# Performance work log

Hardware: AMD Instinct MI355X
Metric: run time of the kernel (lower is better)

## Reference

```python
import jax, jax.numpy as jnp
import numpy as np
import math

N = 50000
E = 800000
HID = 128
HEADS = 8
DK = HID // HEADS
EPS_LN = 1e-5


def setup_inputs() -> dict:
    key = jax.random.key(0)
    ks = jax.random.split(key, 20)
    s = 1.0 / math.sqrt(HID)
    inp = {
        'x': jax.random.normal(ks[0], (N, HID), jnp.float32),
        'Wq': jax.random.normal(ks[1], (HID, HID), jnp.float32) * s,
        'bq': jnp.zeros((HID,), jnp.float32),
        'Wk': jax.random.normal(ks[2], (HID, HID), jnp.float32) * s,
        'bk': jnp.zeros((HID,), jnp.float32),
        'Wv': jax.random.normal(ks[3], (HID, HID), jnp.float32) * s,
        'bv': jnp.zeros((HID,), jnp.float32),
        'Wo': jax.random.normal(ks[4], (HID, HID), jnp.float32) * s,
        'bo': jnp.zeros((HID,), jnp.float32),
        'ln1_g': jnp.ones((HID,), jnp.float32),
        'ln1_b': jnp.zeros((HID,), jnp.float32),
        'W1': jax.random.normal(ks[5], (HID, 4 * HID), jnp.float32) * s,
        'b1': jnp.zeros((4 * HID,), jnp.float32),
        'W2': jax.random.normal(ks[6], (4 * HID, HID), jnp.float32) * (0.5 * s),
        'b2': jnp.zeros((HID,), jnp.float32),
        'ln2_g': jnp.ones((HID,), jnp.float32),
        'ln2_b': jnp.zeros((HID,), jnp.float32),
        'edge_index': jax.random.randint(ks[7], (2, E), 0, N, jnp.int64 if jax.config.jax_enable_x64 else jnp.int32),
    }
    return inp


def _layer_norm(x, g, b):
    mu = jnp.mean(x, axis=-1, keepdims=True)
    var = jnp.mean(jnp.square(x - mu), axis=-1, keepdims=True)
    return (x - mu) * jax.lax.rsqrt(var + EPS_LN) * g + b


def reference(x, Wq, bq, Wk, bk, Wv, bv, Wo, bo, ln1_g, ln1_b, W1, b1, W2, b2, ln2_g, ln2_b, edge_index):
    n = x.shape[0]
    src, tgt = edge_index[0], edge_index[1]
    Q = (x @ Wq + bq).reshape(n, HEADS, DK)
    K = (x @ Wk + bk).reshape(n, HEADS, DK)
    V = (x @ Wv + bv).reshape(n, HEADS, DK)
    # per-edge scores: (E, H)
    scores = jnp.sum(Q[tgt] * K[src], axis=-1) / math.sqrt(DK)
    # segment softmax over incoming edges of each target node
    smax = jax.ops.segment_max(scores, tgt, num_segments=n)  # (N, H), -inf for empty
    sexp = jnp.exp(scores - smax[tgt])
    ssum = jax.ops.segment_sum(sexp, tgt, num_segments=n)
    alpha = sexp / (ssum[tgt] + 1e-16)  # (E, H)
    # weighted V aggregation
    messages = alpha[:, :, None] * V[src]  # (E, H, DK)
    agg = jax.ops.segment_sum(messages, tgt, num_segments=n).reshape(n, HID)
    out = agg @ Wo + bo
    h = _layer_norm(x + out, ln1_g, ln1_b)
    ff = jax.nn.relu(h @ W1 + b1) @ W2 + b2
    return _layer_norm(h + ff, ln2_g, ln2_b)
```

## Files before the change

### kernel.cpp

```cpp
#include <hip/hip_runtime.h>
#include <math.h>

typedef __attribute__((ext_vector_type(8))) short bf16x8;
typedef __attribute__((ext_vector_type(4))) float f32x4;

__device__ __forceinline__ unsigned short f2b(float f) {
    unsigned int u = __float_as_uint(f);
    unsigned int r = (u + 0x7fffu + ((u >> 16) & 1u)) >> 16;
    return (unsigned short)r;
}
__device__ __forceinline__ float blo(unsigned int w) { return __uint_as_float(w << 16); }
__device__ __forceinline__ float bhi(unsigned int w) { return __uint_as_float(w & 0xffff0000u); }
__device__ __forceinline__ float b2f(unsigned short u) { return __uint_as_float((unsigned int)u << 16); }

__device__ __forceinline__ void gload_lds16(const void* g, void* lds) {
    __builtin_amdgcn_global_load_lds(
        (const __attribute__((address_space(1))) unsigned int*)g,
        (__attribute__((address_space(3))) unsigned int*)lds, 16, 0, 0);
}

template<int K, int EPI>
__global__ __launch_bounds__(256)
void mfma_gemm(const unsigned short* __restrict__ A,
               const unsigned short* __restrict__ BT,
               const float* __restrict__ bias,
               const void* __restrict__ res,
               const float* __restrict__ lng,
               const float* __restrict__ lnb,
               void* __restrict__ outv, int M, int NC)
{
    __shared__ unsigned short As[128 * 64];
    __shared__ unsigned short Bs[128 * 64];
    const int tid  = threadIdx.x;
    const int lane = tid & 63;
    const int wid  = tid >> 6;
    const int wr = wid >> 1, wc = wid & 1;
    const int rowBase = blockIdx.x * 128;
    const int colBase = blockIdx.y * 128;

    f32x4 acc[4][4];
#pragma unroll
    for (int i = 0; i < 4; ++i)
#pragma unroll
        for (int j = 0; j < 4; ++j) acc[i][j] = (f32x4)0.f;

    int srow[4], skoff[4];
#pragma unroll
    for (int t = 0; t < 4; ++t) {
        int c = tid + t * 256;
        int r = c >> 3, cc = c & 7;
        srow[t]  = r;
        skoff[t] = ((cc ^ (r & 7)) << 3);
    }

    const int rl = lane & 15;
    const int kh = lane >> 4;

    for (int k0 = 0; k0 < K; k0 += 64) {
#pragma unroll
        for (int t = 0; t < 4; ++t) {
            int c = tid + t * 256;
            gload_lds16(A + (size_t)(rowBase + srow[t]) * K + k0 + skoff[t], &As[c * 8]);
            gload_lds16(BT + (size_t)(colBase + srow[t]) * K + k0 + skoff[t], &Bs[c * 8]);
        }
        __syncthreads();

        bf16x8 a[4][2], b[4][2];
#pragma unroll
        for (int mi = 0; mi < 4; ++mi)
#pragma unroll
            for (int kt = 0; kt < 2; ++kt) {
                a[mi][kt] = *(const bf16x8*)&As[(((wr * 64 + mi * 16 + rl) * 64) + kt * 32 + kh * 8) ^ ((rl & 7) << 3)];
                b[mi][kt] = *(const bf16x8*)&Bs[(((wc * 64 + mi * 16 + rl) * 64) + kt * 32 + kh * 8) ^ ((rl & 7) << 3)];
            }
#pragma unroll
        for (int kt = 0; kt < 2; ++kt)
#pragma unroll
            for (int mi = 0; mi < 4; ++mi)
#pragma unroll
                for (int ni = 0; ni < 4; ++ni)
                    acc[mi][ni] = __builtin_amdgcn_mfma_f32_16x16x32_bf16(a[mi][kt], b[ni][kt], acc[mi][ni], 0, 0, 0);
        __syncthreads();
    }

    if (EPI == 3 || EPI == 4) {
        float* ls = (float*)As;
        float bb[4], gg[4], be[4];
#pragma unroll
        for (int ni = 0; ni < 4; ++ni) {
            int col = wc * 64 + ni * 16 + rl;
            bb[ni] = bias[col];
            gg[ni] = lng[col];
            be[ni] = lnb[col];
        }
#pragma unroll
        for (int mi = 0; mi < 4; ++mi) {
#pragma unroll
            for (int r = 0; r < 4; ++r) {
                int lrow = wr * 64 + mi * 16 + kh * 4 + r;
                int row  = rowBase + lrow;
                float s = 0.f, ss = 0.f;
#pragma unroll
                for (int ni = 0; ni < 4; ++ni) {
                    int col = wc * 64 + ni * 16 + rl;
                    float rr = 0.f;
                    if (row < M) {
                        if (EPI == 3) rr = ((const float*)res)[(size_t)row * 128 + col];
                        else          rr = b2f(((const unsigned short*)res)[(size_t)row * 128 + col]);
                    }
                    float v = acc[mi][ni][r] + bb[ni] + rr;
                    acc[mi][ni][r] = v;
                    s += v; ss += v * v;
                }
#pragma unroll
                for (int off = 1; off < 16; off <<= 1) {
                    s  += __shfl_xor(s,  off, 64);
                    ss += __shfl_xor(ss, off, 64);
                }
                if (rl == 0) {
                    ls[lrow * 2 + wc]       = s;
                    ls[256 + lrow * 2 + wc] = ss;
                }
            }
        }
        __syncthreads();
#pragma unroll
        for (int mi = 0; mi < 4; ++mi) {
#pragma unroll
            for (int r = 0; r < 4; ++r) {
                int lrow = wr * 64 + mi * 16 + kh * 4 + r;
                int row  = rowBase + lrow;
                float s  = ls[lrow * 2] + ls[lrow * 2 + 1];
                float ss = ls[256 + lrow * 2] + ls[256 + lrow * 2 + 1];
                float mean = s * (1.f / 128.f);
                float var  = ss * (1.f / 128.f) - mean * mean;
                float rstd = rsqrtf(var + 1e-5f);
#pragma unroll
                for (int ni = 0; ni < 4; ++ni) {
                    int col = wc * 64 + ni * 16 + rl;
                    float o = (acc[mi][ni][r] - mean) * rstd * gg[ni] + be[ni];
                    if (EPI == 3) {
                        ((unsigned short*)outv)[(size_t)row * 128 + col] = (row < M) ? f2b(o) : (unsigned short)0;
                    } else {
                        if (row < M) ((float*)outv)[(size_t)row * 128 + col] = o;
                    }
                }
            }
        }
    } else {
#pragma unroll
        for (int ni = 0; ni < 4; ++ni) {
            const int col = colBase + wc * 64 + ni * 16 + rl;
            const float bv = bias[col];
#pragma unroll
            for (int mi = 0; mi < 4; ++mi) {
                const int rowb = rowBase + wr * 64 + mi * 16 + kh * 4;
#pragma unroll
                for (int r = 0; r < 4; ++r) {
                    float v = acc[mi][ni][r] + bv;
                    if (EPI == 1) v = fmaxf(v, 0.f);
                    ((unsigned short*)outv)[(size_t)(rowb + r) * NC + col] = f2b(v);
                }
            }
        }
    }
}

__global__ void cast_all(const float* __restrict__ x, unsigned short* __restrict__ xb,
                         int n, int npad, int xblocks,
                         const float* __restrict__ Wq, const float* __restrict__ Wk,
                         const float* __restrict__ Wv, const float* __restrict__ Wo,
                         const float* __restrict__ W1, const float* __restrict__ W2,
                         const float* __restrict__ bq, const float* __restrict__ bk,
                         const float* __restrict__ bv,
                         unsigned short* __restrict__ WcatT, unsigned short* __restrict__ WoT,
                         unsigned short* __restrict__ W1T, unsigned short* __restrict__ W2T,
                         float* __restrict__ bqkv, int* __restrict__ bcnt)
{
    if (blockIdx.x < (unsigned)xblocks) {
        size_t i = ((size_t)blockIdx.x * 256 + threadIdx.x) * 4;
        if (i >= (size_t)npad * 128) return;
        float4 v = make_float4(0.f, 0.f, 0.f, 0.f);
        if (i < (size_t)n * 128) v = *(const float4*)(x + i);
        ushort4 o;
        o.x = f2b(v.x); o.y = f2b(v.y); o.z = f2b(v.z); o.w = f2b(v.w);
        *(ushort4*)(xb + i) = o;
        return;
    }
    int i = (blockIdx.x - xblocks) * 256 + threadIdx.x;
    if (i < 49152) {
        int j = i >> 7, k = i & 127;
        const float* W = (j < 128) ? Wq : ((j < 256) ? Wk : Wv);
        WcatT[i] = f2b(W[k * 128 + (j & 127)]);
    } else if (i < 65536) {
        int t = i - 49152; int j = t >> 7, k = t & 127;
        WoT[t] = f2b(Wo[k * 128 + j]);
    } else if (i < 131072) {
        int t = i - 65536; int j = t >> 7, k = t & 127;
        W1T[t] = f2b(W1[k * 512 + j]);
    } else if (i < 196608) {
        int t = i - 131072; int j = t >> 9, k = t & 511;
        W2T[t] = f2b(W2[k * 128 + j]);
    }
    if (i < 384) bqkv[i] = (i < 128) ? bq[i] : ((i < 256) ? bk[i - 128] : bv[i - 256]);
    if (i < 1024) bcnt[i] = 0;
}

#define EPB 8192

__global__ __launch_bounds__(512)
void bucket_count(const int* __restrict__ tgt, int* __restrict__ bcnt, int E, int nb)
{
    __shared__ int hist[1024];
    int base = blockIdx.x * EPB;
    for (int i = threadIdx.x; i < nb; i += 512) hist[i] = 0;
    __syncthreads();
    int end = min(base + EPB, E);
    for (int e = base + threadIdx.x; e < end; e += 512)
        atomicAdd(&hist[tgt[e] >> 6], 1);
    __syncthreads();
    for (int i = threadIdx.x; i < nb; i += 512)
        if (hist[i] > 0) atomicAdd(&bcnt[i], hist[i]);
}

__global__ __launch_bounds__(64)
void bucket_scan(const int* __restrict__ bcnt, int* __restrict__ bstart,
                 int* __restrict__ bcur, int nb, int E)
{
    int lane = threadIdx.x;
    int carry = 0;
    for (int c = 0; c < nb; c += 64) {
        int idx = c + lane;
        int v = (idx < nb) ? bcnt[idx] : 0;
        int orig = v;
#pragma unroll
        for (int off = 1; off < 64; off <<= 1) {
            int y = __shfl_up(v, off, 64);
            if (lane >= off) v += y;
        }
        if (idx < nb) { int ex = carry + v - orig; bstart[idx] = ex; bcur[idx] = ex; }
        carry += __shfl(v, 63, 64);
    }
    if (lane == 0) bstart[nb] = E;
}

__global__ __launch_bounds__(512)
void bucket_group(const int* __restrict__ src, const int* __restrict__ tgt,
                  int* __restrict__ bcur, int2* __restrict__ stage, int E, int nb)
{
    __shared__ int2 eb[EPB];
    __shared__ int hist[1024], lofs[1024], lcur[1024], gbase[1024];
    int base = blockIdx.x * EPB;
    int tid = threadIdx.x;
    for (int i = tid; i < nb; i += 512) { hist[i] = 0; lcur[i] = 0; }
    __syncthreads();
    int end = min(base + EPB, E);
    for (int e = base + tid; e < end; e += 512)
        atomicAdd(&hist[tgt[e] >> 6], 1);
    __syncthreads();
    if (tid < 64) {
        int carry = 0;
        for (int c = 0; c < nb; c += 64) {
            int idx = c + tid;
            int v = (idx < nb) ? hist[idx] : 0;
            int orig = v;
#pragma unroll
            for (int off = 1; off < 64; off <<= 1) {
                int y = __shfl_up(v, off, 64);
                if (tid >= off) v += y;
            }
            if (idx < nb) lofs[idx] = carry + v - orig;
            carry += __shfl(v, 63, 64);
        }
    }
    __syncthreads();
    for (int e = base + tid; e < end; e += 512) {
        int t = tgt[e], b = t >> 6;
        int r = atomicAdd(&lcur[b], 1);
        eb[lofs[b] + r] = make_int2(src[e], t);
    }
    __syncthreads();
    for (int i = tid; i < nb; i += 512)
        if (hist[i] > 0) gbase[i] = atomicAdd(&bcur[i], hist[i]);
    __syncthreads();
    int cnt = end - base;
    for (int i = tid; i < cnt; i += 512) {
        int2 v = eb[i];
        int b = v.y >> 6;
        stage[gbase[b] + (i - lofs[b])] = v;
    }
}

__global__ __launch_bounds__(256)
void bucket_sort(const int2* __restrict__ stage, const int* __restrict__ bstart,
                 int* __restrict__ rowp, int2* __restrict__ epos, int n, int nb)
{
    __shared__ int2 eb[3072], eb2[3072];
    __shared__ int tcnt[64], tofs[64], tcur[64];
    int b = blockIdx.x;
    int t0 = b << 6;
    if (t0 >= n) return;
    int t1 = min(t0 + 64, n);
    int s0 = bstart[b], s1 = bstart[b + 1];
    int cnt = s1 - s0;
    int tid = threadIdx.x;
    if (tid < 64) { tcnt[tid] = 0; tcur[tid] = 0; }
    __syncthreads();
    bool fits = (cnt <= 3072);
    if (fits) {
        for (int i = tid; i < cnt; i += 256) {
            int2 v = stage[s0 + i];
            eb[i] = v;
            atomicAdd(&tcnt[v.y - t0], 1);
        }
    } else {
        for (int i = tid; i < cnt; i += 256)
            atomicAdd(&tcnt[stage[s0 + i].y - t0], 1);
    }
    __syncthreads();
    if (tid < 64) {
        int v = tcnt[tid], orig = v;
#pragma unroll
        for (int off = 1; off < 64; off <<= 1) {
            int y = __shfl_up(v, off, 64);
            if (tid >= off) v += y;
        }
        tofs[tid] = v - orig;
        int t = t0 + tid;
        if (t < t1) rowp[t] = s0 + v - orig;
        if (t == n - 1) rowp[n] = s1;
    }
    __syncthreads();
    if (fits) {
        for (int i = tid; i < cnt; i += 256) {
            int2 v = eb[i];
            int lt = v.y - t0;
            int r = atomicAdd(&tcur[lt], 1);
            eb2[tofs[lt] + r] = v;
        }
        __syncthreads();
        for (int i = tid; i < cnt; i += 256) epos[s0 + i] = eb2[i];
    } else {
        for (int i = tid; i < cnt; i += 256) {
            int2 v = stage[s0 + i];
            int lt = v.y - t0;
            int r = atomicAdd(&tcur[lt], 1);
            epos[s0 + tofs[lt] + r] = v;
        }
    }
}

#define SCORE_SCALE 0.360673760222241f

__global__ __launch_bounds__(256)
void score_kernel(const unsigned short* __restrict__ qkv, const int2* __restrict__ epos,
                  float* __restrict__ scores, int E)
{
    int gw = (blockIdx.x * 256 + threadIdx.x) >> 4;
    int el = threadIdx.x & 15;
    if (gw >= E) return;
    int2 st = epos[gw];
    uint4 qv = *(const uint4*)(qkv + (size_t)st.y * 384 + el * 8);
    uint4 kv = *(const uint4*)(qkv + (size_t)st.x * 384 + 128 + el * 8);
    float d;
    d  = blo(qv.x) * blo(kv.x) + bhi(qv.x) * bhi(kv.x);
    d += blo(qv.y) * blo(kv.y) + bhi(qv.y) * bhi(kv.y);
    d += blo(qv.z) * blo(kv.z) + bhi(qv.z) * bhi(kv.z);
    d += blo(qv.w) * blo(kv.w) + bhi(qv.w) * bhi(kv.w);
    d += __shfl_xor(d, 1, 64);
    if ((el & 1) == 0)
        scores[(size_t)gw * 8 + (el >> 1)] = d * SCORE_SCALE;
}

__global__ __launch_bounds__(256)
void attn_agg(const unsigned short* __restrict__ qkv, const int* __restrict__ rowp,
              const int2* __restrict__ epos, const float* __restrict__ sc,
              unsigned short* __restrict__ agg, int n, int npad)
{
    int wid  = (blockIdx.x * blockDim.x + threadIdx.x) >> 6;
    int lane = threadIdx.x & 63;
    if (wid >= npad) return;
    if (wid >= n) { *(unsigned int*)(agg + (size_t)wid * 128 + lane * 2) = 0u; return; }

    const int e0 = rowp[wid];
    const int e1 = rowp[wid + 1];

    const int h1 = lane & 7;
    float m = -1e30f, s = 0.f;
    for (int e = e0 + (lane >> 3); e < e1; e += 8) {
        float v = sc[(size_t)e * 8 + h1];
        float mn = fmaxf(m, v);
        s = s * exp2f(m - mn) + exp2f(v - mn);
        m = mn;
    }
#pragma unroll
    for (int off = 8; off < 64; off <<= 1) {
        float mo = __shfl_xor(m, off, 64);
        float so = __shfl_xor(s, off, 64);
        float mn = fmaxf(m, mo);
        s = s * exp2f(m - mn) + so * exp2f(mo - mn);
        m = mn;
    }
    const int head = lane >> 3;
    const float M   = __shfl(m, head, 64);
    const float inv = 1.f / (__shfl(s, head, 64) + 1e-16f);

    float a0 = 0.f, a1 = 0.f;
    int e = e0;
    for (; e + 4 <= e1; e += 4) {
        int s0 = epos[e].x, s1 = epos[e + 1].x, s2 = epos[e + 2].x, s3 = epos[e + 3].x;
        float w0 = exp2f(sc[(size_t)e * 8 + head] - M);
        float w1 = exp2f(sc[(size_t)(e + 1) * 8 + head] - M);
        float w2 = exp2f(sc[(size_t)(e + 2) * 8 + head] - M);
        float w3 = exp2f(sc[(size_t)(e + 3) * 8 + head] - M);
        unsigned int v0 = *(const unsigned int*)(qkv + (size_t)s0 * 384 + 256 + lane * 2);
        unsigned int v1 = *(const unsigned int*)(qkv + (size_t)s1 * 384 + 256 + lane * 2);
        unsigned int v2 = *(const unsigned int*)(qkv + (size_t)s2 * 384 + 256 + lane * 2);
        unsigned int v3 = *(const unsigned int*)(qkv + (size_t)s3 * 384 + 256 + lane * 2);
        a0 += (w0 * blo(v0) + w1 * blo(v1)) + (w2 * blo(v2) + w3 * blo(v3));
        a1 += (w0 * bhi(v0) + w1 * bhi(v1)) + (w2 * bhi(v2) + w3 * bhi(v3));
    }
    for (; e < e1; ++e) {
        int sx = epos[e].x;
        float w = exp2f(sc[(size_t)e * 8 + head] - M);
        unsigned int vw = *(const unsigned int*)(qkv + (size_t)sx * 384 + 256 + lane * 2);
        a0 += w * blo(vw);
        a1 += w * bhi(vw);
    }
    a0 *= inv; a1 *= inv;
    unsigned int o = (unsigned int)f2b(a0) | ((unsigned int)f2b(a1) << 16);
    *(unsigned int*)(agg + (size_t)wid * 128 + lane * 2) = o;
}

extern "C" void kernel_launch(void* const* d_in, const int* in_sizes, int n_in,
                              void* d_out, int out_size, void* d_ws, size_t ws_size,
                              hipStream_t stream)
{
    const float* x    = (const float*)d_in[0];
    const float* Wq   = (const float*)d_in[1];
    const float* bq   = (const float*)d_in[2];
    const float* Wk   = (const float*)d_in[3];
    const float* bk   = (const float*)d_in[4];
    const float* Wv   = (const float*)d_in[5];
    const float* bv   = (const float*)d_in[6];
    const float* Wo   = (const float*)d_in[7];
    const float* bo   = (const float*)d_in[8];
    const float* ln1g = (const float*)d_in[9];
    const float* ln1b = (const float*)d_in[10];
    const float* W1   = (const float*)d_in[11];
    const float* b1   = (const float*)d_in[12];
    const float* W2   = (const float*)d_in[13];
    const float* b2   = (const float*)d_in[14];
    const float* ln2g = (const float*)d_in[15];
    const float* ln2b = (const float*)d_in[16];
    const int*   eidx = (const int*)d_in[17];

    const int N_ = in_sizes[0] / 128;
    const int E_ = in_sizes[17] / 2;
    const int Mpad = ((N_ + 127) / 128) * 128;
    const int nb = (N_ + 63) >> 6;
    const int* srcE = eidx;
    const int* tgtE = eidx + E_;
    float* out = (float*)d_out;

    unsigned short* xb   = (unsigned short*)d_ws;
    unsigned short* qkvb = xb + (size_t)Mpad * 128;
    unsigned short* tb   = xb;
    unsigned short* aggb = qkvb + (size_t)Mpad * 384;
    unsigned short* hb   = aggb + (size_t)Mpad * 128;
    float* scores        = (float*)(hb + (size_t)Mpad * 128);
    unsigned short* WcatT = (unsigned short*)(scores + (size_t)E_ * 8);
    unsigned short* WoT  = WcatT + 384 * 128;
    unsigned short* W1T  = WoT + 128 * 128;
    unsigned short* W2T  = W1T + 512 * 128;
    float* bqkv          = (float*)(W2T + 128 * 512);
    int2* stage          = (int2*)(bqkv + 384);
    int2* epos           = stage + E_;
    int* bcnt   = (int*)(epos + E_);
    int* bstart = bcnt + 1024;
    int* bcur   = bstart + 1025;
    int* rowp   = bcur + 1024;

    const int xblocks = (int)(((size_t)Mpad * 128 / 4 + 255) / 256);
    const int gblocks = (E_ + EPB - 1) / EPB;

    cast_all<<<xblocks + 768, 256, 0, stream>>>(x, xb, N_, Mpad, xblocks,
                                                Wq, Wk, Wv, Wo, W1, W2, bq, bk, bv,
                                                WcatT, WoT, W1T, W2T, bqkv, bcnt);

    mfma_gemm<128, 2><<<dim3(Mpad / 128, 3), 256, 0, stream>>>(
        xb, WcatT, bqkv, nullptr, nullptr, nullptr, qkvb, N_, 384);

    bucket_count<<<gblocks, 512, 0, stream>>>(tgtE, bcnt, E_, nb);
    bucket_scan<<<1, 64, 0, stream>>>(bcnt, bstart, bcur, nb, E_);
    bucket_group<<<gblocks, 512, 0, stream>>>(srcE, tgtE, bcur, stage, E_, nb);
    bucket_sort<<<nb, 256, 0, stream>>>(stage, bstart, rowp, epos, N_, nb);

    score_kernel<<<((size_t)E_ * 16 + 255) / 256, 256, 0, stream>>>(qkvb, epos, scores, E_);
    attn_agg<<<(Mpad + 3) / 4, 256, 0, stream>>>(qkvb, rowp, epos, scores, aggb, N_, Mpad);

    mfma_gemm<128, 3><<<dim3(Mpad / 128, 1), 256, 0, stream>>>(
        aggb, WoT, bo, x, ln1g, ln1b, hb, N_, 128);

    mfma_gemm<128, 1><<<dim3(Mpad / 128, 4), 256, 0, stream>>>(
        hb, W1T, b1, nullptr, nullptr, nullptr, tb, N_, 512);

    mfma_gemm<512, 4><<<dim3(Mpad / 128, 1), 256, 0, stream>>>(
        tb, W2T, b2, hb, ln2g, ln2b, out, N_, 128);
}
```

Before: 222.9 us.

## Precompute unnormalized bf16 exp weights and split edge aggregation across two wavefronts

The score kernel now writes exp2 of the scaled score directly as bf16, without subtracting the max. The aggregation kernel then drops its separate online-softmax pass and accumulates the weight sum alongside the weighted V. Each target node's edges are split between two wavefronts whose partial sums are combined through LDS. This removes a pass over the scores, halves score storage and adds parallelism per node. In exchange it risks overflow or underflow for large scores, since no max is subtracted, and loses precision from storing weights in bf16.

```diff
diff --git a/kernel.cpp b/kernel.cpp
--- a/kernel.cpp
+++ b/kernel.cpp
@@ -354,7 +354,7 @@
 
 __global__ __launch_bounds__(256)
 void score_kernel(const unsigned short* __restrict__ qkv, const int2* __restrict__ epos,
-                  float* __restrict__ scores, int E)
+                  unsigned short* __restrict__ wexp, int E)
 {
     int gw = (blockIdx.x * 256 + threadIdx.x) >> 4;
     int el = threadIdx.x & 15;
@@ -369,67 +369,67 @@
     d += blo(qv.w) * blo(kv.w) + bhi(qv.w) * bhi(kv.w);
     d += __shfl_xor(d, 1, 64);
     if ((el & 1) == 0)
-        scores[(size_t)gw * 8 + (el >> 1)] = d * SCORE_SCALE;
+        wexp[(size_t)gw * 8 + (el >> 1)] = f2b(exp2f(d * SCORE_SCALE));
 }
 
 __global__ __launch_bounds__(256)
 void attn_agg(const unsigned short* __restrict__ qkv, const int* __restrict__ rowp,
-              const int2* __restrict__ epos, const float* __restrict__ sc,
+              const int2* __restrict__ epos, const unsigned short* __restrict__ wexp,
               unsigned short* __restrict__ agg, int n, int npad)
 {
-    int wid  = (blockIdx.x * blockDim.x + threadIdx.x) >> 6;
-    int lane = threadIdx.x & 63;
-    if (wid >= npad) return;
-    if (wid >= n) { *(unsigned int*)(agg + (size_t)wid * 128 + lane * 2) = 0u; return; }
-
-    const int e0 = rowp[wid];
-    const int e1 = rowp[wid + 1];
-
-    const int h1 = lane & 7;
-    float m = -1e30f, s = 0.f;
-    for (int e = e0 + (lane >> 3); e < e1; e += 8) {
-        float v = sc[(size_t)e * 8 + h1];
-        float mn = fmaxf(m, v);
-        s = s * exp2f(m - mn) + exp2f(v - mn);
-        m = mn;
-    }
-#pragma unroll
-    for (int off = 8; off < 64; off <<= 1) {
-        float mo = __shfl_xor(m, off, 64);
-        float so = __shfl_xor(s, off, 64);
-        float mn = fmaxf(m, mo);
-        s = s * exp2f(m - mn) + so * exp2f(mo - mn);
-        m = mn;
-    }
+    __shared__ float ls[2][2][192];
+    const int tid  = threadIdx.x;
+    const int lane = tid & 63;
+    const int half = (tid >> 6) & 1;
+    const int tin  = tid >> 7;
+    const int wid  = blockIdx.x * 2 + tin;
     const int head = lane >> 3;
-    const float M   = __shfl(m, head, 64);
-    const float inv = 1.f / (__shfl(s, head, 64) + 1e-16f);
-
-    float a0 = 0.f, a1 = 0.f;
-    int e = e0;
-    for (; e + 4 <= e1; e += 4) {
-        int s0 = epos[e].x, s1 = epos[e + 1].x, s2 = epos[e + 2].x, s3 = epos[e + 3].x;
-        float w0 = exp2f(sc[(size_t)e * 8 + head] - M);
-        float w1 = exp2f(sc[(size_t)(e + 1) * 8 + head] - M);
-        float w2 = exp2f(sc[(size_t)(e + 2) * 8 + head] - M);
-        float w3 = exp2f(sc[(size_t)(e + 3) * 8 + head] - M);
-        unsigned int v0 = *(const unsigned int*)(qkv + (size_t)s0 * 384 + 256 + lane * 2);
-        unsigned int v1 = *(const unsigned int*)(qkv + (size_t)s1 * 384 + 256 + lane * 2);
-        unsigned int v2 = *(const unsigned int*)(qkv + (size_t)s2 * 384 + 256 + lane * 2);
-        unsigned int v3 = *(const unsigned int*)(qkv + (size_t)s3 * 384 + 256 + lane * 2);
-        a0 += (w0 * blo(v0) + w1 * blo(v1)) + (w2 * blo(v2) + w3 * blo(v3));
-        a1 += (w0 * bhi(v0) + w1 * bhi(v1)) + (w2 * bhi(v2) + w3 * bhi(v3));
-    }
-    for (; e < e1; ++e) {
-        int sx = epos[e].x;
-        float w = exp2f(sc[(size_t)e * 8 + head] - M);
-        unsigned int vw = *(const unsigned int*)(qkv + (size_t)sx * 384 + 256 + lane * 2);
-        a0 += w * blo(vw);
-        a1 += w * bhi(vw);
-    }
-    a0 *= inv; a1 *= inv;
-    unsigned int o = (unsigned int)f2b(a0) | ((unsigned int)f2b(a1) << 16);
-    *(unsigned int*)(agg + (size_t)wid * 128 + lane * 2) = o;
+
+    float s = 0.f, a0 = 0.f, a1 = 0.f;
+    if (wid < n) {
+        const int r0 = rowp[wid], r1 = rowp[wid + 1];
+        const int mid = r0 + ((r1 - r0 + 1) >> 1);
+        int e = half ? mid : r0;
+        const int ee = half ? r1 : mid;
+        for (; e + 4 <= ee; e += 4) {
+            int s0 = epos[e].x, s1 = epos[e + 1].x, s2 = epos[e + 2].x, s3 = epos[e + 3].x;
+            float w0 = b2f(wexp[(size_t)e * 8 + head]);
+            float w1 = b2f(wexp[(size_t)(e + 1) * 8 + head]);
+            float w2 = b2f(wexp[(size_t)(e + 2) * 8 + head]);
+            float w3 = b2f(wexp[(size_t)(e + 3) * 8 + head]);
+            unsigned int v0 = *(const unsigned int*)(qkv + (size_t)s0 * 384 + 256 + lane * 2);
+            unsigned int v1 = *(const unsigned int*)(qkv + (size_t)s1 * 384 + 256 + lane * 2);
+            unsigned int v2 = *(const unsigned int*)(qkv + (size_t)s2 * 384 + 256 + lane * 2);
+            unsigned int v3 = *(const unsigned int*)(qkv + (size_t)s3 * 384 + 256 + lane * 2);
+            s  += (w0 + w1) + (w2 + w3);
+            a0 += (w0 * blo(v0) + w1 * blo(v1)) + (w2 * blo(v2) + w3 * blo(v3));
+            a1 += (w0 * bhi(v0) + w1 * bhi(v1)) + (w2 * bhi(v2) + w3 * bhi(v3));
+        }
+        for (; e < ee; ++e) {
+            int sx = epos[e].x;
+            float w = b2f(wexp[(size_t)e * 8 + head]);
+            unsigned int vw = *(const unsigned int*)(qkv + (size_t)sx * 384 + 256 + lane * 2);
+            s  += w;
+            a0 += w * blo(vw);
+            a1 += w * bhi(vw);
+        }
+    }
+    ls[tin][half][lane * 2]     = a0;
+    ls[tin][half][lane * 2 + 1] = a1;
+    ls[tin][half][128 + lane]   = s;
+    __syncthreads();
+    if (half == 0 && wid < npad) {
+        if (wid >= n) {
+            *(unsigned int*)(agg + (size_t)wid * 128 + lane * 2) = 0u;
+        } else {
+            a0 += ls[tin][1][lane * 2];
+            a1 += ls[tin][1][lane * 2 + 1];
+            s  += ls[tin][1][128 + lane];
+            float inv = 1.f / (s + 1e-16f);
+            unsigned int o = (unsigned int)f2b(a0 * inv) | ((unsigned int)f2b(a1 * inv) << 16);
+            *(unsigned int*)(agg + (size_t)wid * 128 + lane * 2) = o;
+        }
+    }
 }
 
 extern "C" void kernel_launch(void* const* d_in, const int* in_sizes, int n_in,
@@ -468,8 +468,8 @@
     unsigned short* tb   = xb;
     unsigned short* aggb = qkvb + (size_t)Mpad * 384;
     unsigned short* hb   = aggb + (size_t)Mpad * 128;
-    float* scores        = (float*)(hb + (size_t)Mpad * 128);
-    unsigned short* WcatT = (unsigned short*)(scores + (size_t)E_ * 8);
+    unsigned short* wexp = hb + (size_t)Mpad * 128;
+    unsigned short* WcatT = wexp + (size_t)E_ * 8;
     unsigned short* WoT  = WcatT + 384 * 128;
     unsigned short* W1T  = WoT + 128 * 128;
     unsigned short* W2T  = W1T + 512 * 128;
@@ -496,8 +496,8 @@
     bucket_group<<<gblocks, 512, 0, stream>>>(srcE, tgtE, bcur, stage, E_, nb);
     bucket_sort<<<nb, 256, 0, stream>>>(stage, bstart, rowp, epos, N_, nb);
 
-    score_kernel<<<((size_t)E_ * 16 + 255) / 256, 256, 0, stream>>>(qkvb, epos, scores, E_);
-    attn_agg<<<(Mpad + 3) / 4, 256, 0, stream>>>(qkvb, rowp, epos, scores, aggb, N_, Mpad);
+    score_kernel<<<((size_t)E_ * 16 + 255) / 256, 256, 0, stream>>>(qkvb, epos, wexp, E_);
+    attn_agg<<<Mpad / 2, 256, 0, stream>>>(qkvb, rowp, epos, wexp, aggb, N_, Mpad);
 
     mfma_gemm<128, 3><<<dim3(Mpad / 128, 1), 256, 0, stream>>>(
         aggb, WoT, bo, x, ln1g, ln1b, hb, N_, 128);
```

After: 224.6 us. About the same (+0.8%).
